# Optimization experiments

Measured on AMD Instinct MI355X. Metric: run time of the kernel, lower is better.

## Reference

```python
import jax, jax.numpy as jnp
import numpy as np

B, LQ, LK, F = 8, 4096, 4096, 64


def setup_inputs() -> dict:
    key = jax.random.key(0)
    ks = jax.random.split(key, 9)
    s = 1.0 / np.sqrt(F)
    return {
        "query": jax.random.normal(ks[0], (B, LQ, F), dtype=jnp.float32),
        "key": jax.random.normal(ks[1], (B, LK, F), dtype=jnp.float32),
        "value": jax.random.normal(ks[2], (B, LQ, F), dtype=jnp.float32),
        "wq": jax.random.normal(ks[3], (F, F), dtype=jnp.float32) * s,
        "bq": jax.random.normal(ks[4], (F,), dtype=jnp.float32) * 0.01,
        "wk": jax.random.normal(ks[5], (F, F), dtype=jnp.float32) * s,
        "bk": jax.random.normal(ks[6], (F,), dtype=jnp.float32) * 0.01,
        "wv": jax.random.normal(ks[7], (F, F), dtype=jnp.float32) * s,
        "bv": jax.random.normal(ks[8], (F,), dtype=jnp.float32) * 0.01,
    }


def reference(query, key, value, wq, bq, wk, bk, wv, bv):
    # nn.Linear: x @ W.T + b
    q = query @ wq.T + bq          # [B, LQ, F]
    k = key @ wk.T + bk            # [B, LK, F]
    v = value @ wv.T + bv          # [B, LQ, F]
    # scores[b, i, j] = <k_i, q_j>; NO 1/sqrt(d) scaling (faithful to source)
    scores = jnp.einsum('bkf,bqf->bkq', k, q)       # [B, LK, LQ]
    attn = jax.nn.softmax(scores, axis=-1)          # softmax over query positions
    return jnp.einsum('bkq,bqf->bkf', attn, v)      # [B, LK, F]
```

## Files before the change

### kernel.cpp

```cpp
#include <hip/hip_runtime.h>


typedef unsigned short u16;
typedef __attribute__((ext_vector_type(4))) unsigned int u32x4;
typedef __attribute__((ext_vector_type(4))) float f32x4;
typedef __attribute__((ext_vector_type(16))) float f32x16;
typedef __attribute__((ext_vector_type(2))) float f32x2;
typedef __attribute__((ext_vector_type(8))) short s16x8;

#define MFMA32(a, bb, c) __builtin_amdgcn_mfma_f32_32x32x16_bf16((a), (bb), (c), 0, 0, 0)
#define MFMA16(a, bb, c) __builtin_amdgcn_mfma_f32_16x16x32_bf16((a), (bb), (c), 0, 0, 0)

__device__ __forceinline__ short f2bf(float x) {
    unsigned u = __builtin_bit_cast(unsigned, x);
    u += 0x7fffu + ((u >> 16) & 1u);
    return (short)(u >> 16);
}
__device__ __forceinline__ float bf2f(short h) {
    unsigned u = ((unsigned)(u16)h) << 16;
    return __builtin_bit_cast(float, u);
}
__device__ __forceinline__ f32x4 zero4() { f32x4 r = {0.f, 0.f, 0.f, 0.f}; return r; }

__device__ __forceinline__ void split8(f32x4 a, f32x4 b, s16x8& hi, s16x8& lo) {
#pragma unroll
    for (int i = 0; i < 4; i++) {
        short h = f2bf(a[i]);
        hi[i] = h;
        lo[i] = f2bf(a[i] - bf2f(h));
    }
#pragma unroll
    for (int i = 0; i < 4; i++) {
        short h = f2bf(b[i]);
        hi[i + 4] = h;
        lo[i + 4] = f2bf(b[i] - bf2f(h));
    }
}

__global__ __launch_bounds__(256) void proj_qkv_32727650796335(
    const float* __restrict__ q_, const float* __restrict__ k_, const float* __restrict__ v_,
    const float* __restrict__ wq, const float* __restrict__ bq,
    const float* __restrict__ wk, const float* __restrict__ bk,
    const float* __restrict__ wv, const float* __restrict__ bv,
    u16* __restrict__ qph, u16* __restrict__ qpl,
    u16* __restrict__ kph, u16* __restrict__ kpl,
    u16* __restrict__ vp) {
    const int z = blockIdx.y;
    const float* X  = (z == 0) ? q_ : (z == 1) ? k_ : v_;
    const float* W  = (z == 0) ? wq : (z == 1) ? wk : wv;
    const float* bi = (z == 0) ? bq : (z == 1) ? bk : bv;

    const int t = threadIdx.x;
    const int w = t >> 6, ln = t & 63, g = ln >> 4, lq = ln & 15;
    const int cidx = blockIdx.x;

    __shared__ f32x4 ldsX[1024];

    const f32x4* X4 = (const f32x4*)X + (size_t)cidx * 1024;
#pragma unroll
    for (int kk = 0; kk < 4; kk++) {
        int lin = t + 256 * kk;
        int r = lin >> 4, c4 = lin & 15;
        ldsX[r * 16 + (c4 ^ (r & 7))] = X4[lin];
    }
    __syncthreads();

    float bv4[4];
#pragma unroll
    for (int nt = 0; nt < 4; nt++) bv4[nt] = bi[lq + 16 * nt];

    const f32x4* W4 = (const f32x4*)W;
    s16x8 wfh[4][2], wfl[4][2];
#pragma unroll
    for (int nt = 0; nt < 4; nt++)
#pragma unroll
        for (int kb = 0; kb < 2; kb++) {
            f32x4 a = W4[(lq + 16 * nt) * 16 + (g + 8 * kb)];
            f32x4 b = W4[(lq + 16 * nt) * 16 + (g + 4 + 8 * kb)];
            split8(a, b, wfh[nt][kb], wfl[nt][kb]);
        }

    s16x8 afh[2], afl[2];
#pragma unroll
    for (int kb = 0; kb < 2; kb++) {
        f32x4 a = ldsX[(16 * w + lq) * 16 + ((g + 8 * kb) ^ (lq & 7))];
        f32x4 b = ldsX[(16 * w + lq) * 16 + ((g + 4 + 8 * kb) ^ (lq & 7))];
        split8(a, b, afh[kb], afl[kb]);
    }

    f32x4 acc[4];
#pragma unroll
    for (int nt = 0; nt < 4; nt++) acc[nt] = zero4();
#pragma unroll
    for (int kb = 0; kb < 2; kb++)
#pragma unroll
        for (int nt = 0; nt < 4; nt++) {
            acc[nt] = MFMA16(afh[kb], wfh[nt][kb], acc[nt]);
            acc[nt] = MFMA16(afh[kb], wfl[nt][kb], acc[nt]);
            acc[nt] = MFMA16(afl[kb], wfh[nt][kb], acc[nt]);
        }

#pragma unroll
    for (int nt = 0; nt < 4; nt++)
#pragma unroll
        for (int r = 0; r < 4; r++) {
            float val = acc[nt][r] + bv4[nt];
            short hi = f2bf(val);
            short lo = f2bf(val - bf2f(hi));
            int row = 16 * w + 4 * g + r;
            int f = lq + 16 * nt;
            if (z == 1) {
                size_t idx = ((size_t)cidx * 64 + row) * 64 + f;
                kph[idx] = (u16)hi;
                kpl[idx] = (u16)lo;
            } else if (z == 0) {
                unsigned idx = (unsigned)((row >> 5) * 2048 + nt * 512
                             + ((row & 31) + ((lq >> 3) & 1) * 32) * 8 + (lq & 7));
                size_t o = (size_t)cidx * 4096 + idx;
                qph[o] = (u16)hi;
                qpl[o] = (u16)lo;
            } else {
                unsigned idx = (unsigned)((f >> 5) * 2048 + (row >> 4) * 512
                             + ((f & 31) + ((row >> 2) & 1) * 32) * 8
                             + ((row >> 3) & 1) * 4 + (row & 3));
                vp[(size_t)cidx * 4096 + idx] = (u16)hi;
            }
        }
}

__global__ __launch_bounds__(256, 3) void attn_fwd_32727650796335(
    const u16* __restrict__ qph, const u16* __restrict__ qpl,
    const u16* __restrict__ kph, const u16* __restrict__ kpl,
    const u16* __restrict__ vp, float* __restrict__ out,
    float* __restrict__ pO, f32x2* __restrict__ pML, int nsplit) {
    const int t = threadIdx.x;
    const int w = t >> 6, ln = t & 63, i5 = ln & 31, h = ln >> 5;
    const int itile = blockIdx.x, b = blockIdx.y, split = blockIdx.z;
    const int nc = 64 / nsplit;
    const int c0 = split * nc;

    __shared__ u32x4 ldsbuf[1536];
    const char* ldsc = (const char*)ldsbuf;

    const int irow = b * 4096 + itile * 128 + 32 * w + i5;
    const u16* krh = kph + (size_t)irow * 64;
    const u16* krl = kpl + (size_t)irow * 64;
    s16x8 kfh[4], kfl[4];
#pragma unroll
    for (int ks = 0; ks < 4; ks++) {
        kfh[ks] = *(const s16x8*)(krh + 16 * ks + 8 * h);
        kfl[ks] = *(const s16x8*)(krl + 16 * ks + 8 * h);
    }

    f32x16 oacc0 = {}, oacc1 = {};
    float m = -__builtin_inff();
    float lsum = 0.f;

    const u32x4* qsrcH = (const u32x4*)(qph + (size_t)(b * 64) * 4096);
    const u32x4* qsrcL = (const u32x4*)(qpl + (size_t)(b * 64) * 4096);
    const u32x4* vsrc  = (const u32x4*)(vp  + (size_t)(b * 64) * 4096);

    u32x4 qha, qhb, qla, qlb, va, vb;
#define LOADC(c) do { size_t o_ = (size_t)(c) * 512 + t;      \
        qha = qsrcH[o_]; qhb = qsrcH[o_ + 256];               \
        qla = qsrcL[o_]; qlb = qsrcL[o_ + 256];               \
        va  = vsrc[o_];  vb  = vsrc[o_ + 256]; } while (0)

    LOADC(c0);
    for (int cc = 0; cc < nc; cc++) {
        __syncthreads();
        ldsbuf[t] = qha;
        ldsbuf[t + 256] = qhb;
        ldsbuf[t + 512] = qla;
        ldsbuf[t + 768] = qlb;
        ldsbuf[t + 1024] = va;
        ldsbuf[t + 1280] = vb;
        __syncthreads();
        if (cc + 1 < nc) LOADC(c0 + cc + 1);

        f32x16 s0 = {}, s1 = {};
#pragma unroll
        for (int ks = 0; ks < 4; ks++) {
            const int fo = ks * 1024 + ln * 16;
            s16x8 qh0 = *(const s16x8*)(ldsc + fo);
            s16x8 qh1 = *(const s16x8*)(ldsc + 4096 + fo);
            s16x8 ql0 = *(const s16x8*)(ldsc + 8192 + fo);
            s16x8 ql1 = *(const s16x8*)(ldsc + 12288 + fo);
            s0 = MFMA32(qh0, kfh[ks], s0);
            s1 = MFMA32(qh1, kfh[ks], s1);
            s0 = MFMA32(qh0, kfl[ks], s0);
            s1 = MFMA32(qh1, kfl[ks], s1);
            s0 = MFMA32(ql0, kfh[ks], s0);
            s1 = MFMA32(ql1, kfh[ks], s1);
        }

        float pmax = s0[0];
#pragma unroll
        for (int r = 1; r < 16; r++) pmax = fmaxf(pmax, s0[r]);
#pragma unroll
        for (int r = 0; r < 16; r++) pmax = fmaxf(pmax, s1[r]);
        pmax = fmaxf(pmax, __shfl_xor(pmax, 32));
        if (!__all(pmax <= m)) {
            float mnew = fmaxf(m, pmax);
            float corr = __expf(m - mnew);
            lsum *= corr;
#pragma unroll
            for (int r = 0; r < 16; r++) { oacc0[r] *= corr; oacc1[r] *= corr; }
            m = mnew;
        }

        float p0[16], p1[16];
        float psum = 0.f;
#pragma unroll
        for (int r = 0; r < 16; r++) {
            p0[r] = __expf(s0[r] - m);
            p1[r] = __expf(s1[r] - m);
            psum += p0[r] + p1[r];
        }
        psum += __shfl_xor(psum, 32);
        lsum += psum;

        s16x8 pf[4];
#pragma unroll
        for (int qh = 0; qh < 2; qh++)
#pragma unroll
            for (int e = 0; e < 8; e++) {
                pf[qh][e]     = f2bf(p0[8 * qh + e]);
                pf[2 + qh][e] = f2bf(p1[8 * qh + e]);
            }

#pragma unroll
        for (int s4 = 0; s4 < 4; s4++) {
            s16x8 vf0 = *(const s16x8*)(ldsc + 16384 + s4 * 1024 + ln * 16);
            s16x8 vf1 = *(const s16x8*)(ldsc + 16384 + 4096 + s4 * 1024 + ln * 16);
            oacc0 = MFMA32(vf0, pf[s4], oacc0);
            oacc1 = MFMA32(vf1, pf[s4], oacc1);
        }
    }
#undef LOADC

    if (nsplit == 1) {
        float inv = 1.f / lsum;
#pragma unroll
        for (int q = 0; q < 4; q++) {
            f32x4 o0, o1;
#pragma unroll
            for (int r = 0; r < 4; r++) { o0[r] = oacc0[4 * q + r] * inv; o1[r] = oacc1[4 * q + r] * inv; }
            *(f32x4*)(out + (size_t)irow * 64 + 8 * q + 4 * h) = o0;
            *(f32x4*)(out + (size_t)irow * 64 + 32 + 8 * q + 4 * h) = o1;
        }
    } else {
        size_t base = ((size_t)split * 32768 + (size_t)irow) * 64;
#pragma unroll
        for (int q = 0; q < 4; q++) {
            f32x4 o0, o1;
#pragma unroll
            for (int r = 0; r < 4; r++) { o0[r] = oacc0[4 * q + r]; o1[r] = oacc1[4 * q + r]; }
            *(f32x4*)(pO + base + 8 * q + 4 * h) = o0;
            *(f32x4*)(pO + base + 32 + 8 * q + 4 * h) = o1;
        }
        if (ln < 32) {
            f32x2 ml; ml[0] = m; ml[1] = lsum;
            pML[(size_t)split * 32768 + irow] = ml;
        }
    }
}

__global__ __launch_bounds__(256) void combine_32727650796335(
    const float* __restrict__ pO, const f32x2* __restrict__ pML,
    float* __restrict__ out, int nsplit) {
    const int bt = blockIdx.x;
    const int t = threadIdx.x;
    const int row = t >> 2, fb = (t & 3) << 4;
    const size_t grow = (size_t)bt * 64 + row;

    float M = -__builtin_inff();
#pragma unroll
    for (int s = 0; s < 4; s++)
        if (s < nsplit) M = fmaxf(M, pML[(size_t)s * 32768 + grow][0]);

    float wgt0 = 0.f, wgt1 = 0.f, wgt2 = 0.f, wgt3 = 0.f;
    float W = 0.f;
    {
        f32x2 ml;
        ml = pML[grow];                                    wgt0 = __expf(ml[0] - M); W += wgt0 * ml[1];
        if (nsplit > 1) { ml = pML[32768 + grow];          wgt1 = __expf(ml[0] - M); W += wgt1 * ml[1]; }
        if (nsplit > 2) { ml = pML[2 * 32768 + grow];      wgt2 = __expf(ml[0] - M); W += wgt2 * ml[1]; }
        if (nsplit > 3) { ml = pML[3 * 32768 + grow];      wgt3 = __expf(ml[0] - M); W += wgt3 * ml[1]; }
    }
    float inv = 1.f / W;

#pragma unroll
    for (int ff = 0; ff < 16; ff += 4) {
        f32x4 acc = zero4();
        acc += wgt0 * *(const f32x4*)(pO + grow * 64 + fb + ff);
        if (nsplit > 1) acc += wgt1 * *(const f32x4*)(pO + ((size_t)32768 + grow) * 64 + fb + ff);
        if (nsplit > 2) acc += wgt2 * *(const f32x4*)(pO + ((size_t)2 * 32768 + grow) * 64 + fb + ff);
        if (nsplit > 3) acc += wgt3 * *(const f32x4*)(pO + ((size_t)3 * 32768 + grow) * 64 + fb + ff);
        *(f32x4*)(out + grow * 64 + fb + ff) = acc * inv;
    }
}

extern "C" void kernel_launch(void* const* d_in, const int* in_sizes, int n_in,
                              void* d_out, int out_size, void* d_ws, size_t ws_size,
                              hipStream_t stream) {
    (void)in_sizes; (void)n_in; (void)out_size;
    const float* q_ = (const float*)d_in[0];
    const float* k_ = (const float*)d_in[1];
    const float* v_ = (const float*)d_in[2];
    const float* wq = (const float*)d_in[3];
    const float* bq = (const float*)d_in[4];
    const float* wk = (const float*)d_in[5];
    const float* bk = (const float*)d_in[6];
    const float* wv = (const float*)d_in[7];
    const float* bv = (const float*)d_in[8];

    const size_t PLANE = (size_t)8 * 4096 * 64;
    u16* qph = (u16*)d_ws;
    u16* qpl = qph + PLANE;
    u16* kph = qpl + PLANE;
    u16* kpl = kph + PLANE;
    u16* vp  = kpl + PLANE;
    const size_t planes_bytes = 5 * PLANE * sizeof(u16);

    auto fits = [&](int js) {
        size_t need = planes_bytes
                    + (size_t)js * 32768 * 64 * sizeof(float)
                    + (size_t)js * 32768 * sizeof(f32x2);
        return need <= ws_size;
    };
    int nsplit = fits(4) ? 4 : (fits(2) ? 2 : 1);

    float* pO  = (float*)((char*)d_ws + planes_bytes);
    f32x2* pML = (f32x2*)((char*)d_ws + planes_bytes
                          + (size_t)nsplit * 32768 * 64 * sizeof(float));

    proj_qkv_32727650796335<<<dim3(512, 3, 1), 256, 0, stream>>>(
        q_, k_, v_, wq, bq, wk, bk, wv, bv, qph, qpl, kph, kpl, vp);
    attn_fwd_32727650796335<<<dim3(32, 8, nsplit), 256, 0, stream>>>(
        qph, qpl, kph, kpl, vp, (float*)d_out, pO, pML, nsplit);
    if (nsplit > 1)
        combine_32727650796335<<<dim3(512, 1, 1), 256, 0, stream>>>(
            pO, pML, (float*)d_out, nsplit);
}
```

Before: 135.9 us.

## Stage projection outputs through LDS, use exp2 with prescaled keys, raise split count

The projection kernel now writes its bf16 hi/lo tiles into shared memory and copies them out with wide 16-byte stores instead of scattered 2-byte stores. Keys are pre-multiplied by log2(e) so the attention softmax can use the native exp2 instruction instead of __expf. The row max is computed with a tree reduction instead of a serial chain. The split-K count rises to 8 when the workspace allows, which increases grid parallelism but adds more partial-output traffic for the combine kernel to read.

```diff
diff --git a/kernel.cpp b/kernel.cpp
--- a/kernel.cpp
+++ b/kernel.cpp
@@ -10,6 +10,12 @@
 
 #define MFMA32(a, bb, c) __builtin_amdgcn_mfma_f32_32x32x16_bf16((a), (bb), (c), 0, 0, 0)
 #define MFMA16(a, bb, c) __builtin_amdgcn_mfma_f32_16x16x32_bf16((a), (bb), (c), 0, 0, 0)
+
+#if __has_builtin(__builtin_amdgcn_exp2f)
+#define FEXP2(x) __builtin_amdgcn_exp2f(x)
+#else
+#define FEXP2(x) exp2f(x)
+#endif
 
 __device__ __forceinline__ short f2bf(float x) {
     unsigned u = __builtin_bit_cast(unsigned, x);
@@ -55,6 +61,8 @@
     const int cidx = blockIdx.x;
 
     __shared__ f32x4 ldsX[1024];
+    __shared__ __align__(16) u16 outH[4096];
+    __shared__ __align__(16) u16 outLo[4096];
 
     const f32x4* X4 = (const f32x4*)X + (size_t)cidx * 1024;
 #pragma unroll
@@ -105,27 +113,39 @@
 #pragma unroll
         for (int r = 0; r < 4; r++) {
             float val = acc[nt][r] + bv4[nt];
+            if (z == 1) val *= 1.44269504f;
             short hi = f2bf(val);
             short lo = f2bf(val - bf2f(hi));
             int row = 16 * w + 4 * g + r;
             int f = lq + 16 * nt;
-            if (z == 1) {
-                size_t idx = ((size_t)cidx * 64 + row) * 64 + f;
-                kph[idx] = (u16)hi;
-                kpl[idx] = (u16)lo;
-            } else if (z == 0) {
-                unsigned idx = (unsigned)((row >> 5) * 2048 + nt * 512
-                             + ((row & 31) + ((lq >> 3) & 1) * 32) * 8 + (lq & 7));
-                size_t o = (size_t)cidx * 4096 + idx;
-                qph[o] = (u16)hi;
-                qpl[o] = (u16)lo;
+            unsigned idx;
+            if (z == 0) {
+                idx = (unsigned)((row >> 5) * 2048 + nt * 512
+                    + ((row & 31) + ((lq >> 3) & 1) * 32) * 8 + (lq & 7));
+            } else if (z == 1) {
+                idx = (unsigned)(row * 64 + f);
             } else {
-                unsigned idx = (unsigned)((f >> 5) * 2048 + (row >> 4) * 512
-                             + ((f & 31) + ((row >> 2) & 1) * 32) * 8
-                             + ((row >> 3) & 1) * 4 + (row & 3));
-                vp[(size_t)cidx * 4096 + idx] = (u16)hi;
+                idx = (unsigned)((f >> 5) * 2048 + (row >> 4) * 512
+                    + ((f & 31) + ((row >> 2) & 1) * 32) * 8
+                    + ((row >> 3) & 1) * 4 + (row & 3));
             }
-        }
+            outH[idx] = (u16)hi;
+            if (z != 2) outLo[idx] = (u16)lo;
+        }
+    __syncthreads();
+
+    u16* dH = (z == 0) ? qph : (z == 1) ? kph : vp;
+    u32x4* d4 = (u32x4*)(dH + (size_t)cidx * 4096);
+    const u32x4* sH = (const u32x4*)outH;
+    d4[t] = sH[t];
+    d4[t + 256] = sH[t + 256];
+    if (z != 2) {
+        u16* dL = (z == 0) ? qpl : kpl;
+        u32x4* d4l = (u32x4*)(dL + (size_t)cidx * 4096);
+        const u32x4* sL = (const u32x4*)outLo;
+        d4l[t] = sL[t];
+        d4l[t + 256] = sL[t + 256];
+    }
 }
 
 __global__ __launch_bounds__(256, 3) void attn_fwd_32727650796335(
@@ -194,15 +214,19 @@
             s1 = MFMA32(ql1, kfh[ks], s1);
         }
 
-        float pmax = s0[0];
-#pragma unroll
-        for (int r = 1; r < 16; r++) pmax = fmaxf(pmax, s0[r]);
-#pragma unroll
-        for (int r = 0; r < 16; r++) pmax = fmaxf(pmax, s1[r]);
-        pmax = fmaxf(pmax, __shfl_xor(pmax, 32));
+        float mx[16];
+#pragma unroll
+        for (int r = 0; r < 16; r++) mx[r] = fmaxf(s0[r], s1[r]);
+#pragma unroll
+        for (int st = 8; st > 0; st >>= 1)
+#pragma unroll
+            for (int r = 0; r < 8; r++)
+                if (r < st) mx[r] = fmaxf(mx[r], mx[r + st]);
+        float pmax = fmaxf(mx[0], __shfl_xor(mx[0], 32));
+
         if (!__all(pmax <= m)) {
             float mnew = fmaxf(m, pmax);
-            float corr = __expf(m - mnew);
+            float corr = FEXP2(m - mnew);
             lsum *= corr;
 #pragma unroll
             for (int r = 0; r < 16; r++) { oacc0[r] *= corr; oacc1[r] *= corr; }
@@ -213,8 +237,8 @@
         float psum = 0.f;
 #pragma unroll
         for (int r = 0; r < 16; r++) {
-            p0[r] = __expf(s0[r] - m);
-            p1[r] = __expf(s1[r] - m);
+            p0[r] = FEXP2(s0[r] - m);
+            p1[r] = FEXP2(s1[r] - m);
             psum += p0[r] + p1[r];
         }
         psum += __shfl_xor(psum, 32);
@@ -232,7 +256,7 @@
 #pragma unroll
         for (int s4 = 0; s4 < 4; s4++) {
             s16x8 vf0 = *(const s16x8*)(ldsc + 16384 + s4 * 1024 + ln * 16);
-            s16x8 vf1 = *(const s16x8*)(ldsc + 16384 + 4096 + s4 * 1024 + ln * 16);
+            s16x8 vf1 = *(const s16x8*)(ldsc + 20480 + s4 * 1024 + ln * 16);
             oacc0 = MFMA32(vf0, pf[s4], oacc0);
             oacc1 = MFMA32(vf1, pf[s4], oacc1);
         }
@@ -245,7 +269,10 @@
         for (int q = 0; q < 4; q++) {
             f32x4 o0, o1;
 #pragma unroll
-            for (int r = 0; r < 4; r++) { o0[r] = oacc0[4 * q + r] * inv; o1[r] = oacc1[4 * q + r] * inv; }
+            for (int r = 0; r < 4; r++) {
+                o0[r] = oacc0[4 * q + r] * inv;
+                o1[r] = oacc1[4 * q + r] * inv;
+            }
             *(f32x4*)(out + (size_t)irow * 64 + 8 * q + 4 * h) = o0;
             *(f32x4*)(out + (size_t)irow * 64 + 32 + 8 * q + 4 * h) = o1;
         }
@@ -255,7 +282,10 @@
         for (int q = 0; q < 4; q++) {
             f32x4 o0, o1;
 #pragma unroll
-            for (int r = 0; r < 4; r++) { o0[r] = oacc0[4 * q + r]; o1[r] = oacc1[4 * q + r]; }
+            for (int r = 0; r < 4; r++) {
+                o0[r] = oacc0[4 * q + r];
+                o1[r] = oacc1[4 * q + r];
+            }
             *(f32x4*)(pO + base + 8 * q + 4 * h) = o0;
             *(f32x4*)(pO + base + 32 + 8 * q + 4 * h) = o1;
         }
@@ -276,27 +306,28 @@
 
     float M = -__builtin_inff();
 #pragma unroll
-    for (int s = 0; s < 4; s++)
+    for (int s = 0; s < 8; s++)
         if (s < nsplit) M = fmaxf(M, pML[(size_t)s * 32768 + grow][0]);
 
-    float wgt0 = 0.f, wgt1 = 0.f, wgt2 = 0.f, wgt3 = 0.f;
+    float wgt[8];
     float W = 0.f;
-    {
-        f32x2 ml;
-        ml = pML[grow];                                    wgt0 = __expf(ml[0] - M); W += wgt0 * ml[1];
-        if (nsplit > 1) { ml = pML[32768 + grow];          wgt1 = __expf(ml[0] - M); W += wgt1 * ml[1]; }
-        if (nsplit > 2) { ml = pML[2 * 32768 + grow];      wgt2 = __expf(ml[0] - M); W += wgt2 * ml[1]; }
-        if (nsplit > 3) { ml = pML[3 * 32768 + grow];      wgt3 = __expf(ml[0] - M); W += wgt3 * ml[1]; }
+#pragma unroll
+    for (int s = 0; s < 8; s++) {
+        if (s < nsplit) {
+            f32x2 ml = pML[(size_t)s * 32768 + grow];
+            wgt[s] = exp2f(ml[0] - M);
+            W += wgt[s] * ml[1];
+        } else wgt[s] = 0.f;
     }
     float inv = 1.f / W;
 
 #pragma unroll
     for (int ff = 0; ff < 16; ff += 4) {
         f32x4 acc = zero4();
-        acc += wgt0 * *(const f32x4*)(pO + grow * 64 + fb + ff);
-        if (nsplit > 1) acc += wgt1 * *(const f32x4*)(pO + ((size_t)32768 + grow) * 64 + fb + ff);
-        if (nsplit > 2) acc += wgt2 * *(const f32x4*)(pO + ((size_t)2 * 32768 + grow) * 64 + fb + ff);
-        if (nsplit > 3) acc += wgt3 * *(const f32x4*)(pO + ((size_t)3 * 32768 + grow) * 64 + fb + ff);
+#pragma unroll
+        for (int s = 0; s < 8; s++)
+            if (s < nsplit)
+                acc += wgt[s] * *(const f32x4*)(pO + ((size_t)s * 32768 + grow) * 64 + fb + ff);
         *(f32x4*)(out + grow * 64 + fb + ff) = acc * inv;
     }
 }
@@ -329,7 +360,7 @@
                     + (size_t)js * 32768 * sizeof(f32x2);
         return need <= ws_size;
     };
-    int nsplit = fits(4) ? 4 : (fits(2) ? 2 : 1);
+    int nsplit = fits(8) ? 8 : (fits(4) ? 4 : (fits(2) ? 2 : 1));
 
     float* pO  = (float*)((char*)d_ws + planes_bytes);
     f32x2* pML = (f32x2*)((char*)d_ws + planes_bytes
```

After: 158.1 us. +16.3%, slower.
